# Kernel tuning notes

Measured on AMD Instinct MI355X. Metric: run time of the kernel, lower is better.

The kernel has to match this reference:

```python
import jax, jax.numpy as jnp
import numpy as np

DIM = 512
NUM_HEADS = 8
HEAD_DIM = DIM // NUM_HEADS
SR = 2
LN_EPS = 1e-5


def setup_inputs() -> dict:
    key = jax.random.key(0)
    ks = jax.random.split(key, 12)
    B, H, W = 8, 32, 32
    N = H * W
    s = 0.02
    return {
        "x": jax.random.normal(ks[0], (B, N, DIM), jnp.float32),
        "H": H,
        "W": W,
        # weights stored as [in, out] (torch Linear applies x @ W.T + b)
        "q_w": jax.random.normal(ks[1], (DIM, DIM), jnp.float32) * s,
        "q_b": jnp.zeros((DIM,), jnp.float32),
        "kv_w": jax.random.normal(ks[2], (DIM, 2 * DIM), jnp.float32) * s,
        "kv_b": jnp.zeros((2 * DIM,), jnp.float32),
        "sr_w": jax.random.normal(ks[3], (DIM, DIM, SR, SR), jnp.float32) * s,  # OIHW
        "sr_b": jnp.zeros((DIM,), jnp.float32),
        "ln_g": jnp.ones((DIM,), jnp.float32),
        "ln_b": jnp.zeros((DIM,), jnp.float32),
        "proj_w": jax.random.normal(ks[4], (DIM, DIM), jnp.float32) * s,
        "proj_b": jnp.zeros((DIM,), jnp.float32),
    }


def reference(x, H, W, q_w, q_b, kv_w, kv_b, sr_w, sr_b, ln_g, ln_b, proj_w, proj_b):
    B, N, C = x.shape
    hd = HEAD_DIM
    scale = hd ** -0.5

    # q: [B, nh, N, hd]
    q = (x @ q_w + q_b).reshape(B, N, NUM_HEADS, hd).transpose(0, 2, 1, 3)

    # spatial reduction conv (stride=kernel=SR) + LayerNorm
    x2d = x.transpose(0, 2, 1).reshape(B, C, H, W)
    x2d = jax.lax.conv_general_dilated(
        x2d, sr_w, window_strides=(SR, SR), padding="VALID",
        dimension_numbers=("NCHW", "OIHW", "NCHW")) + sr_b[None, :, None, None]
    Nk = x2d.shape[2] * x2d.shape[3]
    x_kv = x2d.reshape(B, C, Nk).transpose(0, 2, 1)  # [B, Nk, C]
    mu = x_kv.mean(-1, keepdims=True)
    var = ((x_kv - mu) ** 2).mean(-1, keepdims=True)
    x_kv = (x_kv - mu) * jax.lax.rsqrt(var + LN_EPS) * ln_g + ln_b

    kv = x_kv @ kv_w + kv_b  # [B, Nk, 2C]
    k, v = kv[..., :C], kv[..., C:]
    # Faithful to torch: reshape folds C/hd into kv-sequence axis -> M = Nk*num_heads,
    # shared (broadcast) across all query heads.
    M = Nk * NUM_HEADS
    k = k.reshape(B, M, hd)
    v = v.reshape(B, M, hd)

    attn = jnp.einsum("bhnd,bmd->bhnm", q, k) * scale  # [B, nh, N, M]
    attn = jax.nn.softmax(attn, axis=-1)
    out = jnp.einsum("bhnm,bmd->bhnd", attn, v)  # [B, nh, N, hd]
    out = out.transpose(0, 2, 1, 3).reshape(B, N, C)
    return out @ proj_w + proj_b
```

## Files before the change

### kernel.cpp

```cpp
#include <hip/hip_runtime.h>
#include <hip/hip_bf16.h>
#include <stdint.h>

typedef __attribute__((ext_vector_type(8))) short short8;
typedef __attribute__((ext_vector_type(4))) float f32x4;

#define MFMA(A, B, C) __builtin_amdgcn_mfma_f32_16x16x32_bf16(A, B, C, 0, 0, 0)

__device__ inline uint32_t bfrne(float f) {
  uint32_t u = __float_as_uint(f);
  return (u + 0x7FFFu + ((u >> 16) & 1u)) >> 16;
}

__device__ inline uint32_t pkrne(float a, float b) {
  union { __hip_bfloat162 v; uint32_t u; } c;
  c.v.x = __float2bfloat16(a);
  c.v.y = __float2bfloat16(b);
  return c.u;
}

__device__ inline float fexp2(float x) { return __builtin_amdgcn_exp2f(x); }

__device__ inline void gload16(const short* g, short* l) {
  __builtin_amdgcn_global_load_lds(
      (const __attribute__((address_space(1))) void*)g,
      (__attribute__((address_space(3))) void*)l, 16, 0, 0);
}

__global__ __launch_bounds__(256) void prep_all_kernel(
    const float* __restrict__ sr_w, const float* __restrict__ kv_w,
    const float* __restrict__ q_w, const float* __restrict__ proj_w,
    const float* __restrict__ x,
    short* __restrict__ WcThi, short* __restrict__ kvThi,
    short* __restrict__ qThi, short* __restrict__ pThi,
    short* __restrict__ xhi) {
  __shared__ float tile[32][33];
  const int blk = blockIdx.x;
  if (blk < 4096) {
    int t = blk * 256 + threadIdx.x;
    int kk = t & 2047, o = t >> 11;
    float v = sr_w[(size_t)o * 2048 + ((kk & 511) << 2) + (kk >> 9)];
    WcThi[t] = (short)bfrne(v);
    return;
  }
  if (blk >= 5120) {
    int t = (blk - 5120) * 256 + threadIdx.x;
    float4 v0 = *(const float4*)&x[(size_t)t * 8];
    float4 v1 = *(const float4*)&x[(size_t)t * 8 + 4];
    uint4 pk;
    pk.x = pkrne(v0.x, v0.y);
    pk.y = pkrne(v0.z, v0.w);
    pk.z = pkrne(v1.x, v1.y);
    pk.w = pkrne(v1.z, v1.w);
    *(uint4*)&xhi[(size_t)t * 8] = pk;
    return;
  }
  const float* in; short* ohi; int N, bx, by;
  if (blk < 4608) {
    in = kv_w; ohi = kvThi; N = 1024;
    int i = blk - 4096; bx = i & 31; by = i >> 5;
  } else if (blk < 4864) {
    in = q_w; ohi = qThi; N = 512;
    int i = blk - 4608; bx = i & 15; by = i >> 4;
  } else {
    in = proj_w; ohi = pThi; N = 512;
    int i = blk - 4864; bx = i & 15; by = i >> 4;
  }
  const int K = 512;
  const int tx = threadIdx.x & 31, ty = threadIdx.x >> 5;
#pragma unroll
  for (int i = 0; i < 4; ++i)
    tile[ty + i * 8][tx] = in[(size_t)(by * 32 + ty + i * 8) * N + bx * 32 + tx];
  __syncthreads();
#pragma unroll
  for (int i = 0; i < 4; ++i) {
    int n = bx * 32 + ty + i * 8;
    float v = tile[tx][ty + i * 8];
    ohi[(size_t)n * K + by * 32 + tx] = (short)bfrne(v);
  }
}

__global__ __launch_bounds__(256) void ln_kernel(
    const float* __restrict__ X, const float* __restrict__ g,
    const float* __restrict__ bta, short* __restrict__ hi) {
  const int row = blockIdx.x, t = threadIdx.x;
  size_t idx = (size_t)row * 512 + t * 2;
  const size_t PS = (size_t)2048 * 512;
  float2 a0 = *(const float2*)&X[idx];
  float2 a1 = *(const float2*)&X[idx + PS];
  float x0 = a0.x + a1.x;
  float x1 = a0.y + a1.y;
  float s = x0 + x1, sq = x0 * x0 + x1 * x1;
#pragma unroll
  for (int off = 1; off < 64; off <<= 1) {
    s += __shfl_xor(s, off);
    sq += __shfl_xor(sq, off);
  }
  __shared__ float rs[4], rq[4];
  int wid = t >> 6;
  if ((t & 63) == 0) { rs[wid] = s; rq[wid] = sq; }
  __syncthreads();
  s = rs[0] + rs[1] + rs[2] + rs[3];
  sq = rq[0] + rq[1] + rq[2] + rq[3];
  float mu = s * (1.f / 512), var = sq * (1.f / 512) - mu * mu;
  float inv = rsqrtf(var + 1e-5f);
  float2 gg = *(const float2*)&g[t * 2], bb = *(const float2*)&bta[t * 2];
  float o0 = (x0 - mu) * inv * gg.x + bb.x;
  float o1 = (x1 - mu) * inv * gg.y + bb.y;
  *(uint32_t*)&hi[idx] = pkrne(o0, o1);
}

template <bool GATHER, int OMODE>
__device__ __forceinline__ void gemm_body(
    short* ldsraw,
    const short* __restrict__ Ahi, const short* __restrict__ BThi,
    const float* __restrict__ bias, float* __restrict__ C,
    short* __restrict__ Chi, short* __restrict__ Vfo, float oscale,
    int M, int N, int lda, int ldb, int klen,
    int bxx, int byy, int bzz) {
  typedef short (*ldsA_t)[64][8];
  typedef short (*ldsB_t)[128][8];
  ldsA_t ldsA = (ldsA_t)ldsraw;
  ldsB_t ldsB = (ldsB_t)(ldsraw + 8 * 64 * 8);
  const int tid = threadIdx.x, lane = tid & 63, wave = tid >> 6;
  const int g = lane >> 4, qi = lane & 15;
  const int row0 = bxx * 64, col0 = byy * 128;
  const int kz = bzz * klen;
  float* Cz = C + (size_t)bzz * M * N;
  const bool dobias = (bzz == 0);
  f32x4 acc[4][2] = {};

  for (int k0 = kz; k0 < kz + klen; k0 += 64) {
    __syncthreads();
#pragma unroll
    for (int r = 0; r < 2; ++r) {
      int c = tid + r * 256;
      int arow = c & 63, akg = c >> 6;
      size_t ao;
      if (GATHER) {
        int row = row0 + arow;
        int bi = row >> 8, p = row & 255;
        int col = k0 + akg * 8;
        int seg = col >> 9, cc = col & 511;
        int n = (2 * (p >> 4) + (seg >> 1)) * 32 + 2 * (p & 15) + (seg & 1);
        ao = ((size_t)bi * 1024 + n) * 512 + cc;
      } else {
        ao = (size_t)(row0 + arow) * lda + k0 + akg * 8;
      }
      gload16(&Ahi[ao], &ldsA[akg][arow][0]);
    }
#pragma unroll
    for (int r = 0; r < 4; ++r) {
      int c = tid + r * 256;
      int bcol = c & 127, bkg = c >> 7;
      size_t bo = (size_t)(col0 + bcol) * ldb + k0 + bkg * 8;
      gload16(&BThi[bo], &ldsB[bkg][bcol][0]);
    }
    __syncthreads();
#pragma unroll
    for (int kk = 0; kk < 2; ++kk) {
      const int kg = kk * 4 + g;
      short8 ah[4], bh[2];
#pragma unroll
      for (int i = 0; i < 4; ++i)
        ah[i] = *(const short8*)&ldsA[kg][i * 16 + qi][0];
#pragma unroll
      for (int j = 0; j < 2; ++j)
        bh[j] = *(const short8*)&ldsB[kg][wave * 32 + j * 16 + qi][0];
#pragma unroll
      for (int i = 0; i < 4; ++i)
#pragma unroll
        for (int j = 0; j < 2; ++j)
          acc[i][j] = MFMA(ah[i], bh[j], acc[i][j]);
    }
  }
#pragma unroll
  for (int i = 0; i < 4; ++i)
#pragma unroll
    for (int j = 0; j < 2; ++j) {
      int colb = col0 + wave * 32 + j * 16 + qi;
      float bs = dobias ? bias[colb] : 0.f;
#pragma unroll
      for (int r = 0; r < 4; ++r) {
        int row = row0 + i * 16 + g * 4 + r;
        if (OMODE == 0) {
          Cz[(size_t)row * N + colb] = acc[i][j][r] + bs;
        } else {
          uint32_t hv = bfrne(acc[i][j][r] + bs);
          int bb2 = row >> 8, p = row & 255;
          if (colb < 512) {
            int m = p * 8 + (colb >> 6), d = colb & 63;
            size_t t = ((((size_t)(bb2 * 32 + (m >> 6)) * 8 +
                          ((m >> 4) & 3) * 2 + (d >> 5)) * 64) +
                        ((d >> 3) & 3) * 16 + (m & 15)) * 8 + (d & 7);
            Chi[t] = (short)hv;
          } else {
            int c2 = colb - 512;
            int m = p * 8 + (c2 >> 6), d = c2 & 63;
            size_t t = ((((size_t)(bb2 * 32 + (m >> 6)) * 8 +
                          ((m >> 5) & 1) * 4 + (d >> 4)) * 64) +
                        ((m >> 3) & 3) * 16 + (d & 15)) * 8 + (m & 7);
            Vfo[t] = (short)hv;
          }
        }
      }
    }
}

template <int OMODE>
__device__ __forceinline__ void gemm_sq_body(
    short* ldsraw,
    const short* __restrict__ Ahi, const short* __restrict__ BThi,
    const float* __restrict__ bias, float* __restrict__ C,
    short* __restrict__ Chi, float oscale,
    int M, int N, int lda, int ldb, int bxx, int byy) {
  typedef short (*lds_t)[128][8];
  lds_t ldsA = (lds_t)ldsraw;
  lds_t ldsB = (lds_t)(ldsraw + 4 * 128 * 8);
  const int tid = threadIdx.x, lane = tid & 63, wave = tid >> 6;
  const int g = lane >> 4, qi = lane & 15;
  const int wr = (wave >> 1) * 64, wc = (wave & 1) * 64;
  const int row0 = bxx * 128, col0 = byy * 128;
  f32x4 acc[4][4] = {};

  for (int k0 = 0; k0 < 512; k0 += 32) {
    __syncthreads();
#pragma unroll
    for (int r = 0; r < 2; ++r) {
      int c = tid + r * 256;
      int arow = c & 127, akg = c >> 7;
      gload16(&Ahi[(size_t)(row0 + arow) * lda + k0 + akg * 8], &ldsA[akg][arow][0]);
      gload16(&BThi[(size_t)(col0 + arow) * ldb + k0 + akg * 8], &ldsB[akg][arow][0]);
    }
    __syncthreads();
    short8 ah[4], bh[4];
#pragma unroll
    for (int i = 0; i < 4; ++i) {
      ah[i] = *(const short8*)&ldsA[g][wr + i * 16 + qi][0];
      bh[i] = *(const short8*)&ldsB[g][wc + i * 16 + qi][0];
    }
#pragma unroll
    for (int i = 0; i < 4; ++i)
#pragma unroll
      for (int j = 0; j < 4; ++j)
        acc[i][j] = MFMA(ah[i], bh[j], acc[i][j]);
  }
#pragma unroll
  for (int i = 0; i < 4; ++i)
#pragma unroll
    for (int j = 0; j < 4; ++j) {
      int colb = col0 + wc + j * 16 + qi;
      float bs = bias[colb];
#pragma unroll
      for (int r = 0; r < 4; ++r) {
        int row = row0 + wr + i * 16 + g * 4 + r;
        if (OMODE == 0) {
          C[(size_t)row * N + colb] = acc[i][j][r] + bs;
        } else {
          Chi[(size_t)row * N + colb] = (short)bfrne((acc[i][j][r] + bs) * oscale);
        }
      }
    }
}

template <int OMODE>
__global__ __launch_bounds__(256) void gemm_sq(
    const short* __restrict__ Ahi, const short* __restrict__ BThi,
    const float* __restrict__ bias, float* __restrict__ C,
    short* __restrict__ Chi, float oscale,
    int M, int N, int lda, int ldb) {
  __shared__ short lds[8192];
  gemm_sq_body<OMODE>(lds, Ahi, BThi, bias, C, Chi, oscale,
                      M, N, lda, ldb, blockIdx.x, blockIdx.y);
}

__global__ __launch_bounds__(256) void conv_q_kernel(
    const short* __restrict__ xhi, const short* __restrict__ WcThi,
    const float* __restrict__ sr_b, float* __restrict__ Cbuf,
    const short* __restrict__ qThi, const float* __restrict__ q_b,
    short* __restrict__ Qhi, float qscale) {
  __shared__ short lds[12288];
  const int blk = blockIdx.x;
  if (blk < 256) {
    int bx = blk & 31, by = (blk >> 5) & 3, bz = blk >> 7;
    gemm_body<true, 0>(lds, xhi, WcThi, sr_b, Cbuf, nullptr, nullptr, 1.f,
                       2048, 512, 512, 2048, 1024, bx, by, bz);
  } else {
    int i = blk - 256;
    int bx = i & 63, by = i >> 6;
    gemm_sq_body<1>(lds, xhi, qThi, q_b, nullptr, Qhi, qscale,
                    8192, 512, 512, 512, bx, by);
  }
}

__global__ __launch_bounds__(256) void kv_gemm_kernel(
    const short* __restrict__ LNhi, const short* __restrict__ kvThi,
    const float* __restrict__ kv_b, short* __restrict__ Kf, short* __restrict__ Vf) {
  __shared__ short lds[12288];
  gemm_body<false, 2>(lds, LNhi, kvThi, kv_b, nullptr, Kf, Vf, 1.f,
                      2048, 1024, 512, 512, 512,
                      blockIdx.x, blockIdx.y, 0);
}

__device__ __forceinline__ void ld8(short8 (&dst)[8], const short* base) {
#pragma unroll
  for (int i = 0; i < 8; ++i)
    dst[i] = *(const short8*)&base[(size_t)i * 512];
}

__device__ __forceinline__ void qk_tile(f32x4 (&s)[2][4], const short8 (&kr)[8],
                                        const short8 (&qh)[2][2]) {
  const f32x4 z = {0.f, 0.f, 0.f, 0.f};
  __builtin_amdgcn_s_setprio(1);
#pragma unroll
  for (int mf = 0; mf < 4; ++mf)
#pragma unroll
    for (int qc = 0; qc < 2; ++qc) {
      s[qc][mf] = MFMA(kr[mf * 2 + 0], qh[qc][0], z);
      s[qc][mf] = MFMA(kr[mf * 2 + 1], qh[qc][1], s[qc][mf]);
    }
  __builtin_amdgcn_s_setprio(0);
}

__device__ __forceinline__ void pack_tile(const f32x4 (&s)[2][4], short* Psw,
                                          int g, int qi, int swz) {
#pragma unroll
  for (int qc = 0; qc < 2; ++qc)
#pragma unroll
    for (int mf = 0; mf < 4; ++mf) {
      uint32_t u0 = __float_as_uint(fexp2(s[qc][mf][0]));
      uint32_t u1 = __float_as_uint(fexp2(s[qc][mf][1]));
      uint32_t u2 = __float_as_uint(fexp2(s[qc][mf][2]));
      uint32_t u3 = __float_as_uint(fexp2(s[qc][mf][3]));
      uint2 hp;
      hp.x = (u0 >> 16) | (u1 & 0xffff0000u);
      hp.y = (u2 >> 16) | (u3 & 0xffff0000u);
      int uw = ((mf * 4 + g) ^ swz) << 2;
      *(uint2*)&Psw[qc * 1024 + qi * 64 + uw] = hp;
    }
}

__device__ __forceinline__ void pv_tile(const short8 (&vr)[8], short* Psw,
                                        f32x4 (&lacc)[2], f32x4 (&oacc)[2][4],
                                        int g, int qi, int swz) {
  const short8 ones = {(short)0x3F80, (short)0x3F80, (short)0x3F80, (short)0x3F80,
                       (short)0x3F80, (short)0x3F80, (short)0x3F80, (short)0x3F80};
#pragma unroll
  for (int qc = 0; qc < 2; ++qc)
#pragma unroll
    for (int ks2 = 0; ks2 < 2; ++ks2) {
      int ur = ((ks2 * 8 + g * 2) ^ swz) << 2;
      short8 pa = *(const short8*)&Psw[qc * 1024 + qi * 64 + ur];
      __builtin_amdgcn_s_setprio(1);
      lacc[qc] = MFMA(ones, pa, lacc[qc]);
#pragma unroll
      for (int df = 0; df < 4; ++df)
        oacc[qc][df] = MFMA(vr[ks2 * 4 + df], pa, oacc[qc][df]);
      __builtin_amdgcn_s_setprio(0);
    }
}

__global__ __launch_bounds__(256, 2) void attn_kernel(
    const short* __restrict__ Qhi, const short* __restrict__ Kf,
    const short* __restrict__ Vf, short* __restrict__ Ohi) {
  __shared__ short Ps[4][2][1024];
  const int tid = threadIdx.x, lane = tid & 63, wave = tid >> 6;
  const int g = lane >> 4, qi = lane & 15;
  const int h = blockIdx.y, b = blockIdx.z;
  const int n0 = blockIdx.x * 128 + wave * 32;
  const int swz = (qi & 7) << 1;
  short* Psw = &Ps[wave][0][0];

  short8 qh[2][2];
#pragma unroll
  for (int qc = 0; qc < 2; ++qc) {
    const size_t qrow = ((size_t)b * 1024 + n0 + qc * 16 + qi) * 512 + h * 64;
#pragma unroll
    for (int ks = 0; ks < 2; ++ks)
      qh[qc][ks] = *(const short8*)&Qhi[qrow + (ks * 4 + g) * 8];
  }
  f32x4 lacc[2] = {};
  f32x4 oacc[2][4] = {};
  const short* Kb = Kf + (size_t)b * 131072 + lane * 8;
  const short* Vb = Vf + (size_t)b * 131072 + lane * 8;

  short8 kA[8], kB[8], vr[8];
  f32x4 sA[2][4], sB[2][4];
  ld8(kA, Kb);
  ld8(kB, Kb + 4096);
  qk_tile(sA, kA, qh);
  for (int t = 0; t < 32; t += 2) {
    const short* tK = Kb + (size_t)t * 4096;
    const short* tV = Vb + (size_t)t * 4096;
    ld8(vr, tV);
    if (t < 30) ld8(kA, tK + 8192);
    pack_tile(sA, Psw, g, qi, swz);
    qk_tile(sB, kB, qh);
    pv_tile(vr, Psw, lacc, oacc, g, qi, swz);
    ld8(vr, tV + 4096);
    if (t < 30) ld8(kB, tK + 12288);
    pack_tile(sB, Psw, g, qi, swz);
    if (t < 30) qk_tile(sA, kA, qh);
    pv_tile(vr, Psw, lacc, oacc, g, qi, swz);
  }
#pragma unroll
  for (int qc = 0; qc < 2; ++qc) {
    float linv = 1.f / lacc[qc][0];
    size_t obase = ((size_t)b * 1024 + n0 + qc * 16 + qi) * 512 + h * 64;
#pragma unroll
    for (int df = 0; df < 4; ++df) {
      float o0 = oacc[qc][df][0] * linv, o1 = oacc[qc][df][1] * linv;
      float o2 = oacc[qc][df][2] * linv, o3 = oacc[qc][df][3] * linv;
      uint2 hp;
      hp.x = pkrne(o0, o1);
      hp.y = pkrne(o2, o3);
      *(uint2*)&Ohi[obase + df * 16 + g * 4] = hp;
    }
  }
}

extern "C" void kernel_launch(void* const* d_in, const int* in_sizes, int n_in,
                              void* d_out, int out_size, void* d_ws, size_t ws_size,
                              hipStream_t stream) {
  const float* x      = (const float*)d_in[0];
  const float* q_w    = (const float*)d_in[3];
  const float* q_b    = (const float*)d_in[4];
  const float* kv_w   = (const float*)d_in[5];
  const float* kv_b   = (const float*)d_in[6];
  const float* sr_w   = (const float*)d_in[7];
  const float* sr_b   = (const float*)d_in[8];
  const float* ln_g   = (const float*)d_in[9];
  const float* ln_b   = (const float*)d_in[10];
  const float* proj_w = (const float*)d_in[11];
  const float* proj_b = (const float*)d_in[12];

  char* W = (char*)d_ws;
  const size_t MB = 1024 * 1024;
  short* xhi   = (short*)(W);
  short* WcThi = (short*)(W + 16 * MB);
  float* Cbuf  = (float*)(W + 20 * MB);
  short* LNhi  = (short*)(W + 36 * MB);
  short* kvThi = (short*)(W + 40 * MB);
  short* qThi  = (short*)(W + 42 * MB);
  short* pThi  = (short*)(W + 43 * MB);
  short* Qhi   = (short*)(W + 44 * MB);
  short* Kf    = (short*)(W + 20 * MB);
  short* Vf    = (short*)(W + 22 * MB);
  short* Ohi   = (short*)(W);

  prep_all_kernel<<<7168, 256, 0, stream>>>(
      sr_w, kv_w, q_w, proj_w, x, WcThi, kvThi, qThi, pThi, xhi);
  conv_q_kernel<<<512, 256, 0, stream>>>(
      xhi, WcThi, sr_b, Cbuf, qThi, q_b, Qhi, 0.125f * 1.44269504f);
  ln_kernel<<<2048, 256, 0, stream>>>(Cbuf, ln_g, ln_b, LNhi);
  kv_gemm_kernel<<<dim3(32, 8), 256, 0, stream>>>(LNhi, kvThi, kv_b, Kf, Vf);
  attn_kernel<<<dim3(8, 8, 8), 256, 0, stream>>>(Qhi, Kf, Vf, Ohi);
  gemm_sq<0><<<dim3(64, 4), 256, 0, stream>>>(
      Ohi, pThi, proj_b, (float*)d_out, nullptr, 1.f, 8192, 512, 512, 512);
}
```

Before: 115.8 us.

## Run conv GEMM on square-tile body with 4-way split-K gather

The strided conv GEMM now runs on the square 128x128 tile body instead of the separate gemm_body. Its A operand is gathered straight from xhi, and K is split four ways with each z-slice writing a partial fp32 buffer. The LayerNorm kernel now sums four partials instead of two, and the K/V buffers move in the workspace to make room for the larger Cbuf. This trades more partial-sum traffic for bigger tiles, a smaller LDS footprint and uniform block shapes with the fused Q projection.

```diff
diff --git a/kernel.cpp b/kernel.cpp
--- a/kernel.cpp
+++ b/kernel.cpp
@@ -88,8 +88,10 @@
   const size_t PS = (size_t)2048 * 512;
   float2 a0 = *(const float2*)&X[idx];
   float2 a1 = *(const float2*)&X[idx + PS];
-  float x0 = a0.x + a1.x;
-  float x1 = a0.y + a1.y;
+  float2 a2 = *(const float2*)&X[idx + 2 * PS];
+  float2 a3 = *(const float2*)&X[idx + 3 * PS];
+  float x0 = a0.x + a1.x + a2.x + a3.x;
+  float x1 = a0.y + a1.y + a2.y + a3.y;
   float s = x0 + x1, sq = x0 * x0 + x1 * x1;
 #pragma unroll
   for (int off = 1; off < 64; off <<= 1) {
@@ -207,13 +209,14 @@
     }
 }
 
-template <int OMODE>
+template <bool GATHER, int OMODE>
 __device__ __forceinline__ void gemm_sq_body(
     short* ldsraw,
     const short* __restrict__ Ahi, const short* __restrict__ BThi,
     const float* __restrict__ bias, float* __restrict__ C,
     short* __restrict__ Chi, float oscale,
-    int M, int N, int lda, int ldb, int bxx, int byy) {
+    int M, int N, int lda, int ldb, int klen,
+    int bxx, int byy, int bzz) {
   typedef short (*lds_t)[128][8];
   lds_t ldsA = (lds_t)ldsraw;
   lds_t ldsB = (lds_t)(ldsraw + 4 * 128 * 8);
@@ -221,15 +224,29 @@
   const int g = lane >> 4, qi = lane & 15;
   const int wr = (wave >> 1) * 64, wc = (wave & 1) * 64;
   const int row0 = bxx * 128, col0 = byy * 128;
+  const int kz = bzz * klen;
+  float* Cz = C + (size_t)bzz * M * N;
+  const bool dobias = (bzz == 0);
   f32x4 acc[4][4] = {};
 
-  for (int k0 = 0; k0 < 512; k0 += 32) {
+  for (int k0 = kz; k0 < kz + klen; k0 += 32) {
     __syncthreads();
 #pragma unroll
     for (int r = 0; r < 2; ++r) {
       int c = tid + r * 256;
       int arow = c & 127, akg = c >> 7;
-      gload16(&Ahi[(size_t)(row0 + arow) * lda + k0 + akg * 8], &ldsA[akg][arow][0]);
+      size_t ao;
+      if (GATHER) {
+        int row = row0 + arow;
+        int bi = row >> 8, p = row & 255;
+        int col = k0 + akg * 8;
+        int seg = col >> 9, cc = col & 511;
+        int n = (2 * (p >> 4) + (seg >> 1)) * 32 + 2 * (p & 15) + (seg & 1);
+        ao = ((size_t)bi * 1024 + n) * 512 + cc;
+      } else {
+        ao = (size_t)(row0 + arow) * lda + k0 + akg * 8;
+      }
+      gload16(&Ahi[ao], &ldsA[akg][arow][0]);
       gload16(&BThi[(size_t)(col0 + arow) * ldb + k0 + akg * 8], &ldsB[akg][arow][0]);
     }
     __syncthreads();
@@ -250,12 +267,12 @@
 #pragma unroll
     for (int j = 0; j < 4; ++j) {
       int colb = col0 + wc + j * 16 + qi;
-      float bs = bias[colb];
+      float bs = dobias ? bias[colb] : 0.f;
 #pragma unroll
       for (int r = 0; r < 4; ++r) {
         int row = row0 + wr + i * 16 + g * 4 + r;
         if (OMODE == 0) {
-          C[(size_t)row * N + colb] = acc[i][j][r] + bs;
+          Cz[(size_t)row * N + colb] = acc[i][j][r] + bs;
         } else {
           Chi[(size_t)row * N + colb] = (short)bfrne((acc[i][j][r] + bs) * oscale);
         }
@@ -263,15 +280,16 @@
     }
 }
 
-template <int OMODE>
+template <bool GATHER, int OMODE>
 __global__ __launch_bounds__(256) void gemm_sq(
     const short* __restrict__ Ahi, const short* __restrict__ BThi,
     const float* __restrict__ bias, float* __restrict__ C,
     short* __restrict__ Chi, float oscale,
-    int M, int N, int lda, int ldb) {
+    int M, int N, int lda, int ldb, int klen) {
   __shared__ short lds[8192];
-  gemm_sq_body<OMODE>(lds, Ahi, BThi, bias, C, Chi, oscale,
-                      M, N, lda, ldb, blockIdx.x, blockIdx.y);
+  gemm_sq_body<GATHER, OMODE>(lds, Ahi, BThi, bias, C, Chi, oscale,
+                              M, N, lda, ldb, klen,
+                              blockIdx.x, blockIdx.y, blockIdx.z);
 }
 
 __global__ __launch_bounds__(256) void conv_q_kernel(
@@ -279,17 +297,17 @@
     const float* __restrict__ sr_b, float* __restrict__ Cbuf,
     const short* __restrict__ qThi, const float* __restrict__ q_b,
     short* __restrict__ Qhi, float qscale) {
-  __shared__ short lds[12288];
+  __shared__ short lds[8192];
   const int blk = blockIdx.x;
   if (blk < 256) {
-    int bx = blk & 31, by = (blk >> 5) & 3, bz = blk >> 7;
-    gemm_body<true, 0>(lds, xhi, WcThi, sr_b, Cbuf, nullptr, nullptr, 1.f,
-                       2048, 512, 512, 2048, 1024, bx, by, bz);
+    int bx = blk & 15, by = (blk >> 4) & 3, bz = blk >> 6;
+    gemm_sq_body<true, 0>(lds, xhi, WcThi, sr_b, Cbuf, nullptr, 1.f,
+                          2048, 512, 512, 2048, 512, bx, by, bz);
   } else {
     int i = blk - 256;
     int bx = i & 63, by = i >> 6;
-    gemm_sq_body<1>(lds, xhi, qThi, q_b, nullptr, Qhi, qscale,
-                    8192, 512, 512, 512, bx, by);
+    gemm_sq_body<false, 1>(lds, xhi, qThi, q_b, nullptr, Qhi, qscale,
+                           8192, 512, 512, 512, 512, bx, by, 0);
   }
 }
 
@@ -444,8 +462,8 @@
   short* qThi  = (short*)(W + 42 * MB);
   short* pThi  = (short*)(W + 43 * MB);
   short* Qhi   = (short*)(W + 44 * MB);
-  short* Kf    = (short*)(W + 20 * MB);
-  short* Vf    = (short*)(W + 22 * MB);
+  short* Kf    = (short*)(W + 16 * MB);
+  short* Vf    = (short*)(W + 18 * MB);
   short* Ohi   = (short*)(W);
 
   prep_all_kernel<<<7168, 256, 0, stream>>>(
@@ -455,6 +473,6 @@
   ln_kernel<<<2048, 256, 0, stream>>>(Cbuf, ln_g, ln_b, LNhi);
   kv_gemm_kernel<<<dim3(32, 8), 256, 0, stream>>>(LNhi, kvThi, kv_b, Kf, Vf);
   attn_kernel<<<dim3(8, 8, 8), 256, 0, stream>>>(Qhi, Kf, Vf, Ohi);
-  gemm_sq<0><<<dim3(64, 4), 256, 0, stream>>>(
-      Ohi, pThi, proj_b, (float*)d_out, nullptr, 1.f, 8192, 512, 512, 512);
-}
+  gemm_sq<false, 0><<<dim3(64, 4, 1), 256, 0, stream>>>(
+      Ohi, pThi, proj_b, (float*)d_out, nullptr, 1.f, 8192, 512, 512, 512, 512);
+}
```

Measured after the change: 117.7 us. No clear change (+1.6%).
